# Performance work log

Measured on AMD Instinct MI355X. Metric: run time of the kernel, lower is better.

Reference implementation:

```python
import jax, jax.numpy as jnp
import numpy as np

B, T, D = 2, 2048, 1024
H, DK, DV, NH = 8, 128, 256, 2  # heads, key dim, value dim (expand_v=2), num_householder
CONV = 4
INTER = 2816
EPS = 1e-6


def rmsnorm(x, w):
    return x * jax.lax.rsqrt(jnp.mean(x * x, -1, keepdims=True) + EPS) * w


def l2norm(x):
    return x * jax.lax.rsqrt(jnp.sum(x * x, -1, keepdims=True) + 1e-6)


def causal_conv_silu(x, w):
    # depthwise causal conv1d with silu activation; x: [B,T,C], w: [C,K]
    K = w.shape[1]
    xp = jnp.pad(x, ((0, 0), (K - 1, 0), (0, 0)))
    y = sum(xp[:, i:i + x.shape[1], :] * w[:, i] for i in range(K))
    return jax.nn.silu(y)


def setup_inputs():
    key = jax.random.key(0)
    ks = jax.random.split(key, 16)
    s = 0.02
    return {
        "hidden_states": jax.random.normal(ks[0], (B, T, D), jnp.float32),
        "attn_norm_w": jnp.ones((D,), jnp.float32),
        "Wq": jax.random.normal(ks[1], (D, H * DK), jnp.float32) * s,
        "Wk": jax.random.normal(ks[2], (D, NH * H * DK), jnp.float32) * s,
        "Wv": jax.random.normal(ks[3], (D, NH * H * DV), jnp.float32) * s,
        "Wb": jax.random.normal(ks[4], (D, H * NH), jnp.float32) * s,
        "Wa": jax.random.normal(ks[5], (D, H), jnp.float32) * s,
        "A_log": jnp.log(jax.random.uniform(ks[6], (H,), jnp.float32, 1.0, 16.0)),
        "dt_bias": jax.random.normal(ks[7], (H,), jnp.float32) * 0.5,
        "conv_q_w": jax.random.normal(ks[8], (H * DK, CONV), jnp.float32) * 0.5,
        "conv_k_w": jax.random.normal(ks[9], (NH * H * DK, CONV), jnp.float32) * 0.5,
        "conv_v_w": jax.random.normal(ks[10], (NH * H * DV, CONV), jnp.float32) * 0.5,
        "Wg": jax.random.normal(ks[11], (D, H * DV), jnp.float32) * s,
        "o_norm_w": jnp.ones((DV,), jnp.float32),
        "Wo": jax.random.normal(ks[12], (H * DV, D), jnp.float32) * s,
        "mlp_norm_w": jnp.ones((D,), jnp.float32),
        "Wgate": jax.random.normal(ks[13], (D, 2 * INTER), jnp.float32) * s,
        "Wdown": jax.random.normal(ks[14], (INTER, D), jnp.float32) * s,
    }


def reference(hidden_states, attn_norm_w, Wq, Wk, Wv, Wb, Wa, A_log, dt_bias,
              conv_q_w, conv_k_w, conv_v_w, Wg, o_norm_w, Wo,
              mlp_norm_w, Wgate, Wdown):
    residual = hidden_states
    x = rmsnorm(hidden_states, attn_norm_w)

    # projections + short conv + silu, then L2-normalized q/k (gated delta rule)
    q = l2norm(causal_conv_silu(x @ Wq, conv_q_w).reshape(B, T, H, DK))
    k = l2norm(causal_conv_silu(x @ Wk, conv_k_w).reshape(B, T, NH, H, DK))
    v = causal_conv_silu(x @ Wv, conv_v_w).reshape(B, T, NH, H, DV)
    beta = jax.nn.sigmoid(x @ Wb).reshape(B, T, H, NH)
    g = -jnp.exp(A_log) * jax.nn.softplus(x @ Wa + dt_bias)  # [B,T,H] log-decay

    def step(S, inp):
        q_t, k_t, v_t, b_t, g_t = inp
        # forget gate applied once per token, then NH Householder delta-rule updates
        S = S * jnp.exp(g_t)[..., None, None]  # S: [B,H,DK,DV]
        for j in range(NH):
            kj, vj, bj = k_t[:, j], v_t[:, j], b_t[..., j]
            kS = jnp.einsum('bhk,bhkv->bhv', kj, S)
            S = S + bj[..., None, None] * jnp.einsum('bhk,bhv->bhkv', kj, vj - kS)
        o_t = jnp.einsum('bhk,bhkv->bhv', q_t, S)
        return S, o_t

    S0 = jnp.zeros((B, H, DK, DV), x.dtype)
    xs = (jnp.swapaxes(q, 0, 1), jnp.swapaxes(k, 0, 1), jnp.swapaxes(v, 0, 1),
          jnp.swapaxes(beta, 0, 1), jnp.swapaxes(g, 0, 1))
    _, o = jax.lax.scan(step, S0, xs)  # [T,B,H,DV]
    o = jnp.swapaxes(o, 0, 1)

    # gated RMSNorm output gate + output projection
    gate = (x @ Wg).reshape(B, T, H, DV)
    o = rmsnorm(o, o_norm_w) * jax.nn.silu(gate)
    hidden = residual + o.reshape(B, T, H * DV) @ Wo

    # GatedMLP (swiglu)
    y = rmsnorm(hidden, mlp_norm_w)
    gate_m, up = jnp.split(y @ Wgate, 2, -1)
    return hidden + (jax.nn.silu(gate_m) * up) @ Wdown
```

## Files before the change

### kernel.cpp

```cpp
#include <hip/hip_runtime.h>
#include <hip/hip_bf16.h>
#include <math.h>

#define Bq 2
#define Tq 2048
#define Dq 1024
#define Hq 8
#define DKq 128
#define DVq 256
#define NHq 2
#define BTq (Bq*Tq)
#define INTERq 2816

typedef __hip_bfloat16 bf16;
typedef short bfv8 __attribute__((ext_vector_type(8)));
typedef float f32v4 __attribute__((ext_vector_type(4)));

__device__ __forceinline__ float b2f(bf16 v){ return __bfloat162float(v); }
__device__ __forceinline__ bf16 f2b(float v){ return __float2bfloat16(v); }
__device__ __forceinline__ float bs2f(short s){
  union { short s; bf16 b; } u; u.s = s; return __bfloat162float(u.b);
}

__device__ __forceinline__ int is_f32(const unsigned* magic){ return magic[0] == 0x3F800000u; }

__device__ __forceinline__ float ldin(const void* p, int f32, size_t i){
  return f32 ? ((const float*)p)[i] : b2f(((const bf16*)p)[i]);
}

__device__ __forceinline__ void gload_lds16(const bf16* g, bf16* lds_uniform){
  __builtin_amdgcn_global_load_lds(
      (const __attribute__((address_space(1))) void*)g,
      (__attribute__((address_space(3))) void*)lds_uniform, 16, 0, 0);
}

__device__ __forceinline__ float wave_sum(float v){
  #pragma unroll
  for (int off = 32; off > 0; off >>= 1) v += __shfl_xor(v, off, 64);
  return v;
}

__device__ __forceinline__ float block_reduce_sum(float v, float* red){
  #pragma unroll
  for (int off = 32; off > 0; off >>= 1) v += __shfl_down(v, off, 64);
  int lane = threadIdx.x & 63, wid = threadIdx.x >> 6;
  if (lane == 0) red[wid] = v;
  __syncthreads();
  int nw = (blockDim.x + 63) >> 6;
  float tot = 0.f;
  for (int i = 0; i < nw; i++) tot += red[i];
  return tot;
}


struct WSplitArgs {
  const void* W[7];
  bf16* hi[7];
  bf16* lo[7];
  int K[7];
  int N[7];
  int il[7];
  int cum[8];
};

__global__ __launch_bounds__(256) void wsplit_all_kernel(WSplitArgs a,
    const unsigned* __restrict__ magic){
  __shared__ float tile[32][33];
  int f32 = is_f32(magic);
  int bid = blockIdx.x;
  int wi = 0;
  #pragma unroll
  for (int i = 1; i < 7; i++) if (bid >= a.cum[i]) wi = i;
  int rem = bid - a.cum[wi];
  const void* W = a.W[wi];
  bf16* hi = a.hi[wi];
  bf16* lo = a.lo[wi];
  int K = a.K[wi], N = a.N[wi], il = a.il[wi];
  int nbx = N >> 5;
  int n0 = (rem % nbx) * 32, k0 = (rem / nbx) * 32;
  int tx = threadIdx.x & 31, ty = threadIdx.x >> 5;
  #pragma unroll
  for (int r = 0; r < 4; r++){
    int kr = ty + r*8;
    tile[kr][tx] = ldin(W, f32, (size_t)(k0 + kr)*N + n0 + tx);
  }
  __syncthreads();
  int NH2 = N >> 1;
  #pragma unroll
  for (int r = 0; r < 4; r++){
    int nl = ty + r*8;
    int nr = n0 + nl;
    float v = tile[tx][nl];
    bf16 h = f2b(v);
    int cp = nr;
    if (il) cp = (nr < NH2) ? (((nr >> 4) << 5) | (nr & 15))
                            : ((((nr - NH2) >> 4) << 5) | 16 | ((nr - NH2) & 15));
    size_t idx = (size_t)cp*K + k0 + tx;
    hi[idx] = h;
    if (f32) lo[idx] = f2b(v - b2f(h));
  }
}

__device__ __forceinline__ void gemm_acc_bf16(const bf16* __restrict__ A,
    const bf16* __restrict__ Bh, int K, size_t bm, size_t bn,
    bf16* As, bf16* Bs, f32v4 (&acc)[4][4]){
  int tid = threadIdx.x;
  int lane = tid & 63, w = tid >> 6;
  int wm = w >> 1, wn = w & 1;
  int l15 = lane & 15, quad = lane >> 4;
  int srow = tid >> 2;
  int scol = (tid & 3) * 8;
  const bf16* Ag = A  + (bm + srow)*(size_t)K + scol;
  const bf16* Bg = Bh + (bn + srow)*(size_t)K + scol;
  int wslot = w * 512;
  int ntiles = K >> 5;
  int aoff = (wm*64 + l15)*32 + quad*8;
  int boff = (wn*64 + l15)*32 + quad*8;

#define STAGE(buf, kt) { \
    const bf16* a0 = Ag + ((size_t)(kt) << 5); \
    const bf16* b0 = Bg + ((size_t)(kt) << 5); \
    gload_lds16(a0,                &As[(buf)*4096 + wslot]); \
    gload_lds16(a0 + 64*(size_t)K, &As[(buf)*4096 + 2048 + wslot]); \
    gload_lds16(b0,                &Bs[(buf)*4096 + wslot]); \
    gload_lds16(b0 + 64*(size_t)K, &Bs[(buf)*4096 + 2048 + wslot]); }

  STAGE(0, 0)
  if (ntiles > 1) STAGE(1, 1)
  for (int t = 0; t < ntiles; ++t){
    if (t + 1 < ntiles) asm volatile("s_waitcnt vmcnt(4)" ::: "memory");
    else                asm volatile("s_waitcnt vmcnt(0)" ::: "memory");
    __builtin_amdgcn_sched_barrier(0);
    __builtin_amdgcn_s_barrier();
    __builtin_amdgcn_sched_barrier(0);
    int cur = t % 3;
    if (t + 2 < ntiles) STAGE((t + 2) % 3, t + 2)
    bfv8 a[4], bb[4];
    #pragma unroll
    for (int mt = 0; mt < 4; mt++)
      a[mt] = *(const bfv8*)(&As[cur*4096 + aoff + mt*16*32]);
    #pragma unroll
    for (int nn = 0; nn < 4; nn++)
      bb[nn] = *(const bfv8*)(&Bs[cur*4096 + boff + nn*16*32]);
    #pragma unroll
    for (int nn = 0; nn < 4; nn++)
      #pragma unroll
      for (int mt = 0; mt < 4; mt++)
        acc[mt][nn] = __builtin_amdgcn_mfma_f32_16x16x32_bf16(a[mt], bb[nn], acc[mt][nn], 0, 0, 0);
  }
#undef STAGE
}

__device__ __forceinline__ void gemm_acc_f32(const bf16* __restrict__ A,
    const bf16* __restrict__ Bh0, const bf16* __restrict__ Bl0,
    int K, size_t bm, size_t bn, f32v4 (&acc)[4][4]){
  int tid = threadIdx.x;
  int lane = tid & 63, w = tid >> 6;
  int wm = w >> 1, wn = w & 1;
  int l15 = lane & 15, quad = lane >> 4;
  const bf16* Ab = A   + (bm + wm*64 + l15)*(size_t)K + quad*8;
  const bf16* Bh = Bh0 + (bn + wn*64 + l15)*(size_t)K + quad*8;
  const bf16* Bl = Bl0 + (bn + wn*64 + l15)*(size_t)K + quad*8;
  for (int k0 = 0; k0 < K; k0 += 32){
    bfv8 a[4];
    #pragma unroll
    for (int mt = 0; mt < 4; mt++)
      a[mt] = *(const bfv8*)(Ab + (size_t)mt*16*K + k0);
    #pragma unroll
    for (int nt = 0; nt < 4; nt++){
      bfv8 bh = *(const bfv8*)(Bh + (size_t)nt*16*K + k0);
      bfv8 bl = *(const bfv8*)(Bl + (size_t)nt*16*K + k0);
      #pragma unroll
      for (int mt = 0; mt < 4; mt++){
        acc[mt][nt] = __builtin_amdgcn_mfma_f32_16x16x32_bf16(a[mt], bh, acc[mt][nt], 0, 0, 0);
        acc[mt][nt] = __builtin_amdgcn_mfma_f32_16x16x32_bf16(a[mt], bl, acc[mt][nt], 0, 0, 0);
      }
    }
  }
}

__global__ __launch_bounds__(256) void gemm_mfma_kernel(
    const bf16* __restrict__ A, const bf16* __restrict__ WThi, const bf16* __restrict__ WTlo,
    const unsigned* __restrict__ magic,
    const void* __restrict__ res, int res_mode,
    void* __restrict__ out, int out_mode,
    int M, int N, int K){
  __shared__ bf16 As[3*128*32];
  __shared__ bf16 Bs[3*128*32];
  int f32 = is_f32(magic);
  int tid = threadIdx.x;
  int lane = tid & 63, w = tid >> 6;
  int wm = w >> 1, wn = w & 1;
  int l15 = lane & 15, quad = lane >> 4;
  size_t bm = (size_t)blockIdx.x * 128, bn = (size_t)blockIdx.y * 128;

  f32v4 acc[4][4];
  #pragma unroll
  for (int mt = 0; mt < 4; mt++)
    #pragma unroll
    for (int nt = 0; nt < 4; nt++) acc[mt][nt] = 0.f;

  if (f32) gemm_acc_f32(A, WThi, WTlo, K, bm, bn, acc);
  else     gemm_acc_bf16(A, WThi, K, bm, bn, As, Bs, acc);

  if (out_mode == 3){
    #pragma unroll
    for (int mt = 0; mt < 4; mt++)
      #pragma unroll
      for (int nt = 0; nt < 4; nt += 2)
        #pragma unroll
        for (int r = 0; r < 4; r++){
          size_t row = bm + wm*64 + mt*16 + quad*4 + r;
          size_t col = (bn >> 1) + wn*32 + (nt >> 1)*16 + l15;
          float g = acc[mt][nt][r], u = acc[mt][nt+1][r];
          ((bf16*)out)[row*INTERq + col] = f2b(g / (1.f + __expf(-g)) * u);
        }
    return;
  }
  #pragma unroll
  for (int mt = 0; mt < 4; mt++)
    #pragma unroll
    for (int nt = 0; nt < 4; nt++)
      #pragma unroll
      for (int r = 0; r < 4; r++){
        size_t row = bm + wm*64 + mt*16 + quad*4 + r;
        size_t col = bn + wn*64 + nt*16 + l15;
        float v = acc[mt][nt][r];
        if (res_mode == 1) v += ldin(res, f32, row*N + col);
        else if (res_mode == 2) v += ((const float*)res)[row*N + col];
        if (out_mode == 0) ((float*)out)[row*N + col] = v;
        else if (out_mode == 1) ((bf16*)out)[row*N + col] = f2b(v);
        else { if (f32) ((float*)out)[row*N + col] = v; else ((bf16*)out)[row*N + col] = f2b(v); }
      }
}

struct QkvgArgs {
  const bf16* bh[4];
  const bf16* bl[4];
  bf16* out[4];
  int N[4];
  int yoff[5];
};

__global__ __launch_bounds__(256) void gemm_qkvg_kernel(
    const bf16* __restrict__ A, QkvgArgs a, const unsigned* __restrict__ magic){
  __shared__ bf16 As[3*128*32];
  __shared__ bf16 Bs[3*128*32];
  int f32 = is_f32(magic);
  int y = blockIdx.y;
  int g = 0;
  #pragma unroll
  for (int i = 1; i < 4; i++) if (y >= a.yoff[i]) g = i;
  size_t bm = (size_t)blockIdx.x * 128;
  size_t bn = (size_t)(y - a.yoff[g]) * 128;
  int N = a.N[g];

  f32v4 acc[4][4];
  #pragma unroll
  for (int mt = 0; mt < 4; mt++)
    #pragma unroll
    for (int nt = 0; nt < 4; nt++) acc[mt][nt] = 0.f;

  if (f32) gemm_acc_f32(A, a.bh[g], a.bl[g], 1024, bm, bn, acc);
  else     gemm_acc_bf16(A, a.bh[g], 1024, bm, bn, As, Bs, acc);

  bf16* out = a.out[g];
  int tid = threadIdx.x;
  int lane = tid & 63, w = tid >> 6;
  int wm = w >> 1, wn = w & 1;
  int l15 = lane & 15, quad = lane >> 4;
  #pragma unroll
  for (int mt = 0; mt < 4; mt++)
    #pragma unroll
    for (int nt = 0; nt < 4; nt++)
      #pragma unroll
      for (int r = 0; r < 4; r++){
        size_t row = bm + wm*64 + mt*16 + quad*4 + r;
        size_t col = bn + wn*64 + nt*16 + l15;
        out[row*N + col] = f2b(acc[mt][nt][r]);
      }
}

__global__ __launch_bounds__(256) void rmsnorm_betag_kernel(
    const void* __restrict__ hs, const void* __restrict__ attn_nw,
    const void* __restrict__ Wb, const void* __restrict__ Wa,
    const void* __restrict__ A_log, const void* __restrict__ dt_bias,
    const unsigned* __restrict__ magic,
    bf16* __restrict__ xout, float* __restrict__ beta, float* __restrict__ eg){
  __shared__ float xs[Dq];
  __shared__ float red[4];
  int f32 = is_f32(magic);
  size_t bt = blockIdx.x;
  int i0 = threadIdx.x * 4;
  float xv[4];
  if (f32){
    float4 v = *(const float4*)((const float*)hs + bt*Dq + i0);
    xv[0]=v.x; xv[1]=v.y; xv[2]=v.z; xv[3]=v.w;
  } else {
    short4 s = *(const short4*)((const bf16*)hs + bt*Dq + i0);
    xv[0]=bs2f(s.x); xv[1]=bs2f(s.y); xv[2]=bs2f(s.z); xv[3]=bs2f(s.w);
  }
  float ss = fmaf(xv[0],xv[0], fmaf(xv[1],xv[1], fmaf(xv[2],xv[2], xv[3]*xv[3])));
  float tot = block_reduce_sum(ss, red);
  float sc = rsqrtf(tot / (float)Dq + 1e-6f);
  bf16 ob[4];
  #pragma unroll
  for (int j = 0; j < 4; j++){
    float xn = xv[j] * sc * ldin(attn_nw, f32, i0 + j);
    ob[j] = f2b(xn);
    xs[i0 + j] = xn;
  }
  *(short4*)(xout + bt*Dq + i0) = *(short4*)ob;
  __syncthreads();

  int wv = threadIdx.x >> 6, lane = threadIdx.x & 63;
  #pragma unroll
  for (int r = 0; r < 6; r++){
    int n = wv*6 + r;
    float a = 0.f;
    if (n < 16){
      #pragma unroll
      for (int e = 0; e < 16; e++){
        int i = lane + 64*e;
        a = fmaf(xs[i], ldin(Wb, f32, (size_t)i*16 + n), a);
      }
    } else {
      int h = n - 16;
      #pragma unroll
      for (int e = 0; e < 16; e++){
        int i = lane + 64*e;
        a = fmaf(xs[i], ldin(Wa, f32, (size_t)i*8 + h), a);
      }
    }
    #pragma unroll
    for (int off = 32; off > 0; off >>= 1) a += __shfl_down(a, off, 64);
    if (lane == 0){
      if (n < 16){
        int h = n >> 1, j = n & 1;
        beta[(bt*Hq + h)*NHq + j] = 1.f / (1.f + expf(-a));
      } else {
        int h = n - 16;
        a += ldin(dt_bias, f32, h);
        float sp = (a > 20.f) ? a : log1pf(expf(a));
        eg[bt*Hq + h] = expf(-expf(ldin(A_log, f32, h)) * sp);
      }
    }
  }
}

__global__ __launch_bounds__(256) void rmsnorm_kernel(const void* __restrict__ in, int in_mode,
    const void* __restrict__ w, const unsigned* __restrict__ magic,
    bf16* __restrict__ out){
  __shared__ float red[4];
  int f32 = is_f32(magic);
  int inf32 = in_mode ? 1 : f32;
  size_t row = blockIdx.x;
  int i0 = threadIdx.x * 4;
  float xv[4];
  if (inf32){
    float4 v = *(const float4*)((const float*)in + row*Dq + i0);
    xv[0]=v.x; xv[1]=v.y; xv[2]=v.z; xv[3]=v.w;
  } else {
    short4 s = *(const short4*)((const bf16*)in + row*Dq + i0);
    xv[0]=bs2f(s.x); xv[1]=bs2f(s.y); xv[2]=bs2f(s.z); xv[3]=bs2f(s.w);
  }
  float ss = fmaf(xv[0],xv[0], fmaf(xv[1],xv[1], fmaf(xv[2],xv[2], xv[3]*xv[3])));
  float tot = block_reduce_sum(ss, red);
  float sc = rsqrtf(tot / (float)Dq + 1e-6f);
  bf16 ob[4];
  #pragma unroll
  for (int j = 0; j < 4; j++) ob[j] = f2b(xv[j] * sc * ldin(w, f32, i0 + j));
  *(short4*)(out + row*Dq + i0) = *(short4*)ob;
}

__global__ __launch_bounds__(64) void conv_qk_kernel(
    const bf16* __restrict__ qpre, const bf16* __restrict__ kpre,
    const void* __restrict__ wq, const void* __restrict__ wk,
    const unsigned* __restrict__ magic,
    float* __restrict__ qn, float* __restrict__ kn){
  int f32 = is_f32(magic);
  int bt = blockIdx.x;
  int t = bt & (Tq - 1);
  int yb = blockIdx.y;
  const bf16* in; const void* w; int C, cb; float* outf;
  if (yb < 8){ in = qpre; w = wq; C = 1024; cb = yb;     outf = qn; }
  else       { in = kpre; w = wk; C = 2048; cb = yb - 8; outf = kn; }
  int c = cb*128 + threadIdx.x*2;
  float a0 = 0.f, a1 = 0.f;
  #pragma unroll
  for (int i = 0; i < 4; i++){
    int tt = t - 3 + i;
    if (tt >= 0){
      short2 s = *(const short2*)(in + (size_t)(bt - 3 + i)*C + c);
      a0 = fmaf(bs2f(s.x), ldin(w, f32, (size_t)c*4 + i), a0);
      a1 = fmaf(bs2f(s.y), ldin(w, f32, (size_t)(c+1)*4 + i), a1);
    }
  }
  float y0 = a0 / (1.f + __expf(-a0));
  float y1 = a1 / (1.f + __expf(-a1));
  float tot = wave_sum(fmaf(y0, y0, y1*y1));
  float sc = rsqrtf(tot + 1e-6f);
  *(float2*)(outf + (size_t)bt*C + c) = make_float2(y0*sc, y1*sc);
}

__global__ __launch_bounds__(256) void conv_v_kernel(
    const bf16* __restrict__ in, const void* __restrict__ w,
    const unsigned* __restrict__ magic, bf16* __restrict__ out){
  int f32 = is_f32(magic);
  int bt = blockIdx.x;
  int t = bt & (Tq - 1);
  int c = blockIdx.y * 2048 + threadIdx.x * 8;
  float wv[32];
  #pragma unroll
  for (int j = 0; j < 8; j++)
    #pragma unroll
    for (int i = 0; i < 4; i++) wv[j*4+i] = ldin(w, f32, (size_t)(c+j)*4 + i);
  float acc[8] = {0,0,0,0,0,0,0,0};
  #pragma unroll
  for (int i = 0; i < 4; i++){
    int tt = t - 3 + i;
    if (tt >= 0){
      bfv8 v = *(const bfv8*)(in + (size_t)(bt - 3 + i)*4096 + c);
      #pragma unroll
      for (int j = 0; j < 8; j++) acc[j] = fmaf(bs2f(v[j]), wv[j*4+i], acc[j]);
    }
  }
  bf16 ob[8];
  #pragma unroll
  for (int j = 0; j < 8; j++) ob[j] = f2b(acc[j] / (1.f + __expf(-acc[j])));
  *(bfv8*)(out + (size_t)bt*4096 + c) = *(bfv8*)ob;
}

#define DPP_ADD(x, ctrl) ((x) + __int_as_float(__builtin_amdgcn_update_dpp( \
    0, __float_as_int(x), (ctrl), 0xF, 0xF, true)))
#define KRED(p) { p = DPP_ADD(p, 0x128); p = DPP_ADD(p, 0x124); \
                  p = DPP_ADD(p, 0x122); p = DPP_ADD(p, 0x121); }

__global__ __launch_bounds__(64, 1) void scan_kernel(
    const float* __restrict__ qn,
    const float* __restrict__ kn,
    const bf16*  __restrict__ vcv,
    const float* __restrict__ beta,
    const float* __restrict__ eg,
    float* __restrict__ o){
  int bh = blockIdx.x;
  int b = bh >> 3, h = bh & 7;
  int lane = threadIdx.x;
  int kg = lane & 15;
  int vloc = lane >> 4;
  int vv = blockIdx.y * 4 + vloc;
  int c0 = (h << 8) + vv;
  int c1 = 2048 + (h << 8) + vv;
  const size_t base = (size_t)b * Tq;
  const float* knh = kn + base*2048 + h*DKq + kg*8;
  const float* qnh = qn + (base*Hq + h)*(size_t)DKq + kg*8;
  const bf16*  vph = vcv + base*4096;
  const float* gh  = eg + base*Hq + h;
  const float2* bph = (const float2*)(beta + (base*Hq + h)*(size_t)NHq);
  float* oh = o + (base*Hq + h)*(size_t)DVq + vv;

  float4 S0 = {0,0,0,0}, S1 = {0,0,0,0};
#define SDOT(Ka, Kb, p) { \
    float e0 = fmaf(Ka.x, S0.x, Ka.y * S0.y); \
    float e1 = fmaf(Ka.z, S0.z, Ka.w * S0.w); \
    float e2 = fmaf(Kb.x, S1.x, Kb.y * S1.y); \
    float e3 = fmaf(Kb.z, S1.z, Kb.w * S1.w); \
    p = (e0 + e1) + (e2 + e3); }
#define SUPD(Ka, Kb, d) { \
    S0.x = fmaf(Ka.x, d, S0.x); S0.y = fmaf(Ka.y, d, S0.y); \
    S0.z = fmaf(Ka.z, d, S0.z); S0.w = fmaf(Ka.w, d, S0.w); \
    S1.x = fmaf(Kb.x, d, S1.x); S1.y = fmaf(Kb.y, d, S1.y); \
    S1.z = fmaf(Kb.z, d, S1.z); S1.w = fmaf(Kb.w, d, S1.w); }

  float4 A0E = *(const float4*)(knh);
  float4 A1E = *(const float4*)(knh + 4);
  float4 B0E = *(const float4*)(knh + 1024);
  float4 B1E = *(const float4*)(knh + 1028);
  float4 Q0E = *(const float4*)(qnh);
  float4 Q1E = *(const float4*)(qnh + 4);
  float4 A0O = *(const float4*)(knh + 2048);
  float4 A1O = *(const float4*)(knh + 2052);
  float4 B0O = *(const float4*)(knh + 3072);
  float4 B1O = *(const float4*)(knh + 3076);
  float4 Q0O = *(const float4*)(qnh + 1024);
  float4 Q1O = *(const float4*)(qnh + 1028);
  float  gE  = gh[0],   gO  = gh[8];
  float2 beE = bph[0],  beO = bph[8];
  float vaE = b2f(vph[c0]),        vbE = b2f(vph[c1]);
  float vaO = b2f(vph[4096 + c0]), vbO = b2f(vph[4096 + c1]);

#define STEP(A0,A1,B0,B1,Q0,Q1, gS, beS, vaS, vbS, t, tp) { \
    float egv = gS; \
    gS = gh[(tp)*8]; \
    S0.x *= egv; S0.y *= egv; S0.z *= egv; S0.w *= egv; \
    S1.x *= egv; S1.y *= egv; S1.z *= egv; S1.w *= egv; \
    { float p; SDOT(A0, A1, p) \
      KRED(p) \
      float delta = beS.x * (vaS - p); \
      SUPD(A0, A1, delta) \
      A0 = *(const float4*)(knh + (tp)*2048); \
      A1 = *(const float4*)(knh + (tp)*2048 + 4); \
      vaS = b2f(vph[(tp)*4096 + c0]); } \
    { float p; SDOT(B0, B1, p) \
      KRED(p) \
      float delta = beS.y * (vbS - p); \
      SUPD(B0, B1, delta) \
      B0 = *(const float4*)(knh + (tp)*2048 + 1024); \
      B1 = *(const float4*)(knh + (tp)*2048 + 1028); \
      vbS = b2f(vph[(tp)*4096 + c1]); } \
    beS = bph[(tp)*8]; \
    { float p; SDOT(Q0, Q1, p) \
      KRED(p) \
      if ((lane & 15) == 0) oh[(t)*2048] = p; \
      Q0 = *(const float4*)(qnh + (tp)*1024); \
      Q1 = *(const float4*)(qnh + (tp)*1024 + 4); } \
    __builtin_amdgcn_sched_barrier(0); }

  for (int t = 0; t < Tq; t += 2){
    STEP(A0E,A1E,B0E,B1E,Q0E,Q1E, gE,beE,vaE,vbE, t,   t+2)
    STEP(A0O,A1O,B0O,B1O,Q0O,Q1O, gO,beO,vaO,vbO, t+1, t+3)
  }
#undef STEP
#undef SDOT
#undef SUPD
}

__global__ __launch_bounds__(64) void gate_o_kernel(
    const float* __restrict__ o, const void* __restrict__ onw,
    const unsigned* __restrict__ magic,
    const bf16* __restrict__ gate, bf16* __restrict__ og){
  int f32 = is_f32(magic);
  size_t bth = blockIdx.x;
  int d0 = threadIdx.x * 4;
  float4 v = *(const float4*)(o + bth*DVq + d0);
  float tot = wave_sum(fmaf(v.x,v.x, fmaf(v.y,v.y, fmaf(v.z,v.z, v.w*v.w))));
  float sc = rsqrtf(tot / (float)DVq + 1e-6f);
  short4 gs = *(const short4*)(gate + bth*DVq + d0);
  float gv[4] = {bs2f(gs.x), bs2f(gs.y), bs2f(gs.z), bs2f(gs.w)};
  float vv[4] = {v.x, v.y, v.z, v.w};
  bf16 ob[4];
  #pragma unroll
  for (int j = 0; j < 4; j++){
    float silu = gv[j] / (1.f + __expf(-gv[j]));
    ob[j] = f2b(vv[j] * sc * ldin(onw, f32, d0 + j) * silu);
  }
  *(short4*)(og + bth*DVq + d0) = *(short4*)ob;
}

extern "C" void kernel_launch(void* const* d_in, const int* in_sizes, int n_in,
                              void* d_out, int out_size, void* d_ws, size_t ws_size,
                              hipStream_t stream){
  const void* hs      = d_in[0];
  const unsigned* magic = (const unsigned*)d_in[1];
  const void* attn_nw = d_in[1];
  const void* Wq      = d_in[2];
  const void* Wk      = d_in[3];
  const void* Wv      = d_in[4];
  const void* Wb      = d_in[5];
  const void* Wa      = d_in[6];
  const void* A_log   = d_in[7];
  const void* dt_bias = d_in[8];
  const void* conv_q  = d_in[9];
  const void* conv_k  = d_in[10];
  const void* conv_v  = d_in[11];
  const void* Wg      = d_in[12];
  const void* o_nw    = d_in[13];
  const void* Wo      = d_in[14];
  const void* mlp_nw  = d_in[15];
  const void* Wgate   = d_in[16];
  const void* Wdown   = d_in[17];

  char* ws = (char*)d_ws;
  const size_t MB = (size_t)1 << 20;
  size_t X     = 0;
  size_t QPRE  = 8*MB;
  size_t KPRE  = 16*MB;
  size_t VPRE  = 32*MB;
  size_t GATE  = 64*MB;
  size_t QN    = 80*MB;
  size_t KN    = 96*MB;
  size_t HID   = 128*MB;
  size_t BETA  = 144*MB;
  size_t Gb    = 144*MB + 512*1024;
  size_t VCV    = 0;
  size_t O      = 32*MB;
  size_t OG     = QN;
  size_t Y      = KN;
  size_t MID    = O;
  size_t W0 = 145*MB;
  size_t WTQh = W0 +  0*MB, WTQl = W0 +  2*MB;
  size_t WTKh = W0 +  4*MB, WTKl = W0 +  8*MB;
  size_t WTVh = W0 + 12*MB, WTVl = W0 + 20*MB;
  size_t WTGh = W0 + 28*MB, WTGl = W0 + 32*MB;
  size_t WTOh = W0 + 36*MB, WTOl = W0 + 40*MB;
  size_t WTUh = W0 + 44*MB, WTUl = W0 + 56*MB;
  size_t WTDh = W0 + 68*MB, WTDl = W0 + 74*MB;
  (void)ws_size; (void)in_sizes; (void)n_in; (void)out_size;

  WSplitArgs wa;
  {
    const void* Ws[7]  = {Wq, Wk, Wv, Wg, Wo, Wgate, Wdown};
    size_t hio[7]      = {WTQh, WTKh, WTVh, WTGh, WTOh, WTUh, WTDh};
    size_t loo[7]      = {WTQl, WTKl, WTVl, WTGl, WTOl, WTUl, WTDl};
    int Ks[7]          = {1024, 1024, 1024, 1024, 2048, 1024, 2816};
    int Ns[7]          = {1024, 2048, 4096, 2048, 1024, 5632, 1024};
    int ils[7]         = {0, 0, 0, 0, 0, 1, 0};
    int cums[8]        = {0, 1024, 3072, 7168, 9216, 11264, 16896, 19712};
    for (int i = 0; i < 7; i++){
      wa.W[i] = Ws[i]; wa.hi[i] = (bf16*)(ws + hio[i]); wa.lo[i] = (bf16*)(ws + loo[i]);
      wa.K[i] = Ks[i]; wa.N[i] = Ns[i]; wa.il[i] = ils[i]; wa.cum[i] = cums[i];
    }
    wa.cum[7] = cums[7];
    wsplit_all_kernel<<<19712, 256, 0, stream>>>(wa, magic);
  }

  rmsnorm_betag_kernel<<<BTq, 256, 0, stream>>>(hs, attn_nw, Wb, Wa, A_log, dt_bias,
      magic, (bf16*)(ws+X), (float*)(ws+BETA), (float*)(ws+Gb));

  QkvgArgs qa;
  {
    size_t bho[4] = {WTQh, WTKh, WTVh, WTGh};
    size_t blo[4] = {WTQl, WTKl, WTVl, WTGl};
    size_t oo[4]  = {QPRE, KPRE, VPRE, GATE};
    int Ns[4]     = {1024, 2048, 4096, 2048};
    int yo[5]     = {0, 8, 24, 56, 72};
    for (int i = 0; i < 4; i++){
      qa.bh[i] = (const bf16*)(ws + bho[i]); qa.bl[i] = (const bf16*)(ws + blo[i]);
      qa.out[i] = (bf16*)(ws + oo[i]); qa.N[i] = Ns[i]; qa.yoff[i] = yo[i];
    }
    qa.yoff[4] = yo[4];
    gemm_qkvg_kernel<<<dim3(32, 72), 256, 0, stream>>>((const bf16*)(ws+X), qa, magic);
  }

  conv_qk_kernel<<<dim3(BTq, 24), 64, 0, stream>>>((const bf16*)(ws+QPRE), (const bf16*)(ws+KPRE),
      conv_q, conv_k, magic, (float*)(ws+QN), (float*)(ws+KN));
  conv_v_kernel<<<dim3(BTq, 2), 256, 0, stream>>>((const bf16*)(ws+VPRE), conv_v, magic, (bf16*)(ws+VCV));

  scan_kernel<<<dim3(Bq*Hq, DVq/4), 64, 0, stream>>>(
      (const float*)(ws+QN), (const float*)(ws+KN), (const bf16*)(ws+VCV),
      (const float*)(ws+BETA), (const float*)(ws+Gb), (float*)(ws+O));

  gate_o_kernel<<<BTq*Hq, 64, 0, stream>>>((const float*)(ws+O), o_nw, magic,
      (const bf16*)(ws+GATE), (bf16*)(ws+OG));

  gemm_mfma_kernel<<<dim3(32, 8), 256, 0, stream>>>((bf16*)(ws+OG), (bf16*)(ws+WTOh), (bf16*)(ws+WTOl),
      magic, hs, 1, ws+HID, 0, BTq, 1024, 2048);

  rmsnorm_kernel<<<BTq, 256, 0, stream>>>(ws+HID, 1, mlp_nw, magic, (bf16*)(ws+Y));

  gemm_mfma_kernel<<<dim3(32, 44), 256, 0, stream>>>((bf16*)(ws+Y), (bf16*)(ws+WTUh), (bf16*)(ws+WTUl),
      magic, nullptr, 0, ws+MID, 3, BTq, 5632, 1024);

  gemm_mfma_kernel<<<dim3(32, 8), 256, 0, stream>>>((bf16*)(ws+MID), (bf16*)(ws+WTDh), (bf16*)(ws+WTDl),
      magic, ws+HID, 2, d_out, 2, BTq, 1024, 2816);
}
```

Baseline: 2.354 ms.

## Break serial delta-rule chain by precomputing key/query cross dot products

The recurrence step is rewritten algebraically. The three projections of S (k0, k1, q) are computed from the decayed state at once, then corrected with precomputed scalars k1·k0, q·k0 and q·k1. Those cross products for the next token are computed off the critical path, after its inputs load. This removes two dependent reduce-then-update rounds per token, shortening the serial latency chain. In exchange it adds three extra dot products and reductions per step and changes floating-point summation order.

```diff
diff --git a/kernel.cpp b/kernel.cpp
--- a/kernel.cpp
+++ b/kernel.cpp
@@ -51,7 +51,6 @@
   for (int i = 0; i < nw; i++) tot += red[i];
   return tot;
 }
-
 
 struct WSplitArgs {
   const void* W[7];
@@ -466,11 +465,12 @@
     float e2 = fmaf(Kb.x, S1.x, Kb.y * S1.y); \
     float e3 = fmaf(Kb.z, S1.z, Kb.w * S1.w); \
     p = (e0 + e1) + (e2 + e3); }
-#define SUPD(Ka, Kb, d) { \
-    S0.x = fmaf(Ka.x, d, S0.x); S0.y = fmaf(Ka.y, d, S0.y); \
-    S0.z = fmaf(Ka.z, d, S0.z); S0.w = fmaf(Ka.w, d, S0.w); \
-    S1.x = fmaf(Kb.x, d, S1.x); S1.y = fmaf(Kb.y, d, S1.y); \
-    S1.z = fmaf(Kb.z, d, S1.z); S1.w = fmaf(Kb.w, d, S1.w); }
+#define XDOT(Xa, Xb, Ya, Yb, p) { \
+    float e0 = fmaf(Xa.x, Ya.x, Xa.y * Ya.y); \
+    float e1 = fmaf(Xa.z, Ya.z, Xa.w * Ya.w); \
+    float e2 = fmaf(Xb.x, Yb.x, Xb.y * Yb.y); \
+    float e3 = fmaf(Xb.z, Yb.z, Xb.w * Yb.w); \
+    p = (e0 + e1) + (e2 + e3); }
 
   float4 A0E = *(const float4*)(knh);
   float4 A1E = *(const float4*)(knh + 4);
@@ -488,41 +488,58 @@
   float2 beE = bph[0],  beO = bph[8];
   float vaE = b2f(vph[c0]),        vbE = b2f(vph[c1]);
   float vaO = b2f(vph[4096 + c0]), vbO = b2f(vph[4096 + c1]);
-
-#define STEP(A0,A1,B0,B1,Q0,Q1, gS, beS, vaS, vbS, t, tp) { \
+  float c01E, cq0E, cq1E;
+  XDOT(B0E, B1E, A0E, A1E, c01E) KRED(c01E)
+  XDOT(Q0E, Q1E, A0E, A1E, cq0E) KRED(cq0E)
+  XDOT(Q0E, Q1E, B0E, B1E, cq1E) KRED(cq1E)
+  float c01O = 0.f, cq0O = 0.f, cq1O = 0.f;
+
+#define STEP(A0,A1,B0,B1,Q0,Q1, gS, beS, vaS, vbS, c01,cq0,cq1, \
+             AN0,AN1,BN0,BN1,QN0,QN1, c01N,cq0N,cq1N, t, tp) { \
     float egv = gS; \
     gS = gh[(tp)*8]; \
     S0.x *= egv; S0.y *= egv; S0.z *= egv; S0.w *= egv; \
     S1.x *= egv; S1.y *= egv; S1.z *= egv; S1.w *= egv; \
-    { float p; SDOT(A0, A1, p) \
-      KRED(p) \
-      float delta = beS.x * (vaS - p); \
-      SUPD(A0, A1, delta) \
-      A0 = *(const float4*)(knh + (tp)*2048); \
-      A1 = *(const float4*)(knh + (tp)*2048 + 4); \
-      vaS = b2f(vph[(tp)*4096 + c0]); } \
-    { float p; SDOT(B0, B1, p) \
-      KRED(p) \
-      float delta = beS.y * (vbS - p); \
-      SUPD(B0, B1, delta) \
-      B0 = *(const float4*)(knh + (tp)*2048 + 1024); \
-      B1 = *(const float4*)(knh + (tp)*2048 + 1028); \
-      vbS = b2f(vph[(tp)*4096 + c1]); } \
+    float p0, p1r, pq; \
+    SDOT(A0, A1, p0) \
+    SDOT(B0, B1, p1r) \
+    SDOT(Q0, Q1, pq) \
+    KRED(p0) KRED(p1r) KRED(pq) \
+    float d0 = beS.x * (vaS - p0); \
+    float d1 = beS.y * (vbS - fmaf(d0, c01, p1r)); \
+    if ((lane & 15) == 0) oh[(t)*2048] = fmaf(d1, cq1, fmaf(d0, cq0, pq)); \
+    S0.x = fmaf(B0.x, d1, fmaf(A0.x, d0, S0.x)); \
+    S0.y = fmaf(B0.y, d1, fmaf(A0.y, d0, S0.y)); \
+    S0.z = fmaf(B0.z, d1, fmaf(A0.z, d0, S0.z)); \
+    S0.w = fmaf(B0.w, d1, fmaf(A0.w, d0, S0.w)); \
+    S1.x = fmaf(B1.x, d1, fmaf(A1.x, d0, S1.x)); \
+    S1.y = fmaf(B1.y, d1, fmaf(A1.y, d0, S1.y)); \
+    S1.z = fmaf(B1.z, d1, fmaf(A1.z, d0, S1.z)); \
+    S1.w = fmaf(B1.w, d1, fmaf(A1.w, d0, S1.w)); \
+    A0 = *(const float4*)(knh + (tp)*2048); \
+    A1 = *(const float4*)(knh + (tp)*2048 + 4); \
+    B0 = *(const float4*)(knh + (tp)*2048 + 1024); \
+    B1 = *(const float4*)(knh + (tp)*2048 + 1028); \
+    Q0 = *(const float4*)(qnh + (tp)*1024); \
+    Q1 = *(const float4*)(qnh + (tp)*1024 + 4); \
+    vaS = b2f(vph[(tp)*4096 + c0]); \
+    vbS = b2f(vph[(tp)*4096 + c1]); \
     beS = bph[(tp)*8]; \
-    { float p; SDOT(Q0, Q1, p) \
-      KRED(p) \
-      if ((lane & 15) == 0) oh[(t)*2048] = p; \
-      Q0 = *(const float4*)(qnh + (tp)*1024); \
-      Q1 = *(const float4*)(qnh + (tp)*1024 + 4); } \
+    XDOT(BN0, BN1, AN0, AN1, c01N) \
+    XDOT(QN0, QN1, AN0, AN1, cq0N) \
+    XDOT(QN0, QN1, BN0, BN1, cq1N) \
+    KRED(c01N) KRED(cq0N) KRED(cq1N) \
     __builtin_amdgcn_sched_barrier(0); }
 
   for (int t = 0; t < Tq; t += 2){
-    STEP(A0E,A1E,B0E,B1E,Q0E,Q1E, gE,beE,vaE,vbE, t,   t+2)
-    STEP(A0O,A1O,B0O,B1O,Q0O,Q1O, gO,beO,vaO,vbO, t+1, t+3)
+    STEP(A0E,A1E,B0E,B1E,Q0E,Q1E, gE,beE,vaE,vbE, c01E,cq0E,cq1E,
+         A0O,A1O,B0O,B1O,Q0O,Q1O, c01O,cq0O,cq1O, t,   t+2)
+    STEP(A0O,A1O,B0O,B1O,Q0O,Q1O, gO,beO,vaO,vbO, c01O,cq0O,cq1O,
+         A0E,A1E,B0E,B1E,Q0E,Q1E, c01E,cq0E,cq1E, t+1, t+3)
   }
 #undef STEP
 #undef SDOT
-#undef SUPD
+#undef XDOT
 }
 
 __global__ __launch_bounds__(64) void gate_o_kernel(
```

After: 2.713 ms. 15.2% more time.
